# Optimization experiments

Measured on AMD Instinct MI355X. Metric: run time of the kernel, lower is better.

The kernel has to match this reference:

```python
import jax, jax.numpy as jnp
import numpy as np

N = 100_000   # nodes
E = 1_600_000 # edges (avg degree 16)
D0, D1, D2 = 128, 64, 64


def _linp(key, n_out, n_in):
    kw, kb = jax.random.split(key)
    s = 1.0 / np.sqrt(n_in)
    W = jax.random.uniform(kw, (n_out, n_in), jnp.float32, -s, s)
    b = jax.random.uniform(kb, (n_out,), jnp.float32, -s, s)
    return W, b


def setup_inputs() -> dict:
    key = jax.random.key(0)
    ks = jax.random.split(key, 9)
    h = jax.random.normal(ks[0], (N, D0), jnp.float32)
    # guarantee every row has at least one edge (avoids empty-row softmax / 0-std NaNs)
    rows = jnp.concatenate([jnp.arange(N, dtype=jnp.int32),
                            jax.random.randint(ks[1], (E - N,), 0, N, jnp.int32)])
    cols = jax.random.randint(ks[2], (E,), 0, N, jnp.int32)
    edge_index = jnp.stack([rows, cols])  # [2, E], row = softmax segment
    W11, b11 = _linp(ks[3], D1, D0)
    W12, b12 = _linp(ks[4], 1, D1)
    W13, b13 = _linp(ks[5], D1, D0)
    W21, b21 = _linp(ks[6], D2, D1)
    W22, b22 = _linp(ks[7], 1, D2)
    W23, b23 = _linp(ks[8], D2, D1)
    return dict(h=h, edge_index=edge_index,
                W11=W11, b11=b11, W12=W12, b12=b12, W13=W13, b13=b13,
                W21=W21, b21=b21, W22=W22, b22=b22, W23=W23, b23=b23)


def reference(h, edge_index, W11, b11, W12, b12, W13, b13,
              W21, b21, W22, b22, W23, b23):
    src, dst = edge_index[0], edge_index[1]

    def gat_layer(x, Wa, ba, We, be, Wv, bv):
        a = jnp.tanh(x @ Wa.T + ba)                       # [N, d] node scores (l11/l21)
        e = jnp.tanh((a[src] + a[dst]) @ We.T + be)[:, 0] # [E] per-edge logit (l12/l22)
        # per-row (segment) softmax over src = row index
        m = jax.ops.segment_max(e, src, num_segments=N)
        ex = jnp.exp(e - m[src])
        denom = jax.ops.segment_sum(ex, src, num_segments=N)
        att = ex / denom[src]                             # [E]
        v = jnp.tanh(x @ Wv.T + bv)                       # [N, d] values (l13/l23)
        out = jax.ops.segment_sum(att[:, None] * v[dst], src, num_segments=N)  # sparse mm
        return out / jnp.std(out, -1, keepdims=True, ddof=1)  # torch.std is unbiased

    h = gat_layer(h, W11, b11, W12, b12, W13, b13)
    h = gat_layer(h, W21, b21, W22, b22, W23, b23)
    return h
```

## Files before the change

kernel.cpp:

```cpp
#include <hip/hip_runtime.h>


#define WS_ALIGN 256
#define BIN_SHIFT 7
#define BIN_NODES 128
#define BIN_CAP 2560
#define MAX_BINS 1024
#define EPB 4096
#define AGGR_BLOCKS 2048

typedef __attribute__((ext_vector_type(8))) short short8;
typedef __attribute__((ext_vector_type(4))) short short4_t;
typedef __attribute__((ext_vector_type(4))) float f32x4;

__device__ __forceinline__ float fast_tanh(float x) {
  x = fminf(15.f, fmaxf(-15.f, x));
  float e = __expf(2.f * x);
  return (e - 1.f) * __builtin_amdgcn_rcpf(e + 1.f);
}

__device__ __forceinline__ unsigned short f32_to_bf16_rne(float f) {
  unsigned u = __float_as_uint(f);
  unsigned r = u + 0x7fffu + ((u >> 16) & 1u);
  return (unsigned short)(r >> 16);
}

__device__ __forceinline__ void prepw_one(const float* __restrict__ Wa,
                                          const float* __restrict__ Wv,
                                          short* __restrict__ Wh, short* __restrict__ Wl,
                                          int K, int i) {
  int KBLK = K / 32;
  int j = i & 7;
  int c = (i >> 3) & 15;
  int q = (i >> 7) & 3;
  int r = i >> 9;
  int nt = r / KBLK, kb = r - nt * KBLK;
  int row = nt * 16 + c;
  int col = kb * 32 + q * 8 + j;
  float f = (row < 64) ? Wa[row * K + col] : Wv[(row - 64) * K + col];
  unsigned u = __float_as_uint(f);
  float hf = __uint_as_float(u & 0xffff0000u);
  Wh[i] = (short)(u >> 16);
  Wl[i] = (short)(__float_as_uint(f - hf) >> 16);
}

__global__ void k_setup(const float* __restrict__ W11, const float* __restrict__ W13,
                        short* __restrict__ Wh1, short* __restrict__ Wl1,
                        const float* __restrict__ W21, const float* __restrict__ W23,
                        short* __restrict__ Wh2, short* __restrict__ Wl2,
                        int* __restrict__ cursor, int nb) {
  int i = blockIdx.x * 256 + threadIdx.x;
  if (i < 16384) {
    prepw_one(W11, W13, Wh1, Wl1, 128, i);
  } else if (i < 16384 + 8192) {
    prepw_one(W21, W23, Wh2, Wl2, 64, i - 16384);
  } else {
    int b = i - 24576;
    if (b < nb) cursor[b] = b * BIN_CAP;
  }
}

__global__ __launch_bounds__(256) void k_bin(const int* __restrict__ src,
                                             const int* __restrict__ dst,
                                             int* __restrict__ cursor,
                                             int* __restrict__ binned, int E, int nb) {
  __shared__ int ssrc[EPB];
  __shared__ int sdst[EPB];
  __shared__ int hist[MAX_BINS];
  __shared__ int base[MAX_BINS];
  int t = threadIdx.x;
  for (int i = t; i < nb; i += 256) hist[i] = 0;
  __syncthreads();
  int e0 = blockIdx.x * EPB;
  for (int i = t; i < EPB; i += 256) {
    int e = e0 + i;
    int sv = -1, dv = 0;
    if (e < E) {
      sv = src[e];
      dv = dst[e];
      atomicAdd(&hist[sv >> BIN_SHIFT], 1);
    }
    ssrc[i] = sv;
    sdst[i] = dv;
  }
  __syncthreads();
  for (int b = t; b < nb; b += 256) {
    int c = hist[b];
    base[b] = c ? atomicAdd(&cursor[b], c) : 0;
    hist[b] = 0;
  }
  __syncthreads();
  for (int i = t; i < EPB; i += 256) {
    int sv = ssrc[i];
    if (sv >= 0) {
      int b = sv >> BIN_SHIFT;
      int r = atomicAdd(&hist[b], 1);
      int pos = base[b] + r;
      if (pos < (b + 1) * BIN_CAP)
        binned[pos] = (sdst[i] << BIN_SHIFT) | (sv & (BIN_NODES - 1));
    }
  }
}

__global__ __launch_bounds__(256) void k_sort_bin(int* __restrict__ binned,
                                                  const int* __restrict__ cursor,
                                                  int* __restrict__ rs,
                                                  int* __restrict__ re, int n) {
  __shared__ int ents[BIN_CAP];
  __shared__ int sorted[BIN_CAP];
  __shared__ int hist[BIN_NODES];
  __shared__ int scan[BIN_NODES];
  __shared__ int cur[BIN_NODES];
  int bin = blockIdx.x;
  int t = threadIdx.x;
  int nbase = bin << BIN_SHIFT;
  int cnt = cursor[bin] - bin * BIN_CAP;
  if (cnt > BIN_CAP) cnt = BIN_CAP;
  if (t < BIN_NODES) hist[t] = 0;
  __syncthreads();
  int* bp = binned + (size_t)bin * BIN_CAP;
  for (int i = t; i < cnt; i += 256) {
    int pk = bp[i];
    ents[i] = pk;
    atomicAdd(&hist[pk & (BIN_NODES - 1)], 1);
  }
  __syncthreads();
  if (t < BIN_NODES) scan[t] = hist[t];
  __syncthreads();
  for (int off = 1; off < BIN_NODES; off <<= 1) {
    int add = (t < BIN_NODES && t >= off) ? scan[t - off] : 0;
    __syncthreads();
    if (t < BIN_NODES) scan[t] += add;
    __syncthreads();
  }
  if (t < BIN_NODES) {
    int ex = scan[t] - hist[t];
    cur[t] = ex;
    int node = nbase + t;
    if (node < n) {
      rs[node] = bin * BIN_CAP + ex;
      re[node] = bin * BIN_CAP + ex + hist[t];
    }
  }
  __syncthreads();
  for (int i = t; i < cnt; i += 256) {
    int pk = ents[i];
    int pos = atomicAdd(&cur[pk & (BIN_NODES - 1)], 1);
    sorted[pos] = pk;
  }
  __syncthreads();
  for (int i = t; i < cnt; i += 256) {
    int pk = sorted[i];
    int node = pk & (BIN_NODES - 1);
    int hi = scan[node];
    int lo = hi - hist[node];
    int r = lo;
    for (int j = lo; j < hi; j++) {
      int pj = sorted[j];
      r += (pj < pk) || (pj == pk && j < i);
    }
    ents[r] = pk >> BIN_SHIFT;
  }
  __syncthreads();
  for (int i = t; i < cnt; i += 256) bp[i] = ents[i];
}

template <int K>
__global__ __launch_bounds__(256) void k_node(
    const float* __restrict__ x, const short* __restrict__ Wh,
    const short* __restrict__ Wl, const float* __restrict__ ba,
    const float* __restrict__ we, const float* __restrict__ bv,
    unsigned short* __restrict__ v_out, float* __restrict__ s_out, int n) {
  constexpr int KBLK = K / 32;
  constexpr int RS = K + 8;
  __shared__ short sah[64 * RS];
  __shared__ short sal[64 * RS];
  __shared__ float sP[2][64];
  int t = threadIdx.x;
  int l = t & 63;
  int w = t >> 6;
  int q = l >> 4, c = l & 15;
  int node0b = blockIdx.x * 64;

  {
    const float4* xg = (const float4*)(x + (size_t)node0b * K);
    constexpr int R4 = K / 4;
#pragma unroll
    for (int it = 0; it < 64 * R4 / 256; it++) {
      int i = it * 256 + t;
      int r = i / R4, k4 = i - r * R4;
      float4 val = (node0b + r < n) ? xg[i] : (float4){0.f, 0.f, 0.f, 0.f};
      float xv[4] = {val.x, val.y, val.z, val.w};
      short4_t hi, lo;
#pragma unroll
      for (int j = 0; j < 4; j++) {
        unsigned u = __float_as_uint(xv[j]);
        hi[j] = (short)(u >> 16);
        float hf = __uint_as_float(u & 0xffff0000u);
        lo[j] = (short)(__float_as_uint(xv[j] - hf) >> 16);
      }
      *(short4_t*)&sah[r * RS + k4 * 4] = hi;
      *(short4_t*)&sal[r * RS + k4 * 4] = lo;
    }
  }

  const short8* WhF = (const short8*)Wh;
  const short8* WlF = (const short8*)Wl;
  short8 wfh[2][KBLK], wfl[2][KBLK];
#pragma unroll
  for (int mt = 0; mt < 2; mt++)
#pragma unroll
    for (int kb = 0; kb < KBLK; kb++) {
      size_t f = (size_t)((2 * w + mt) * KBLK + kb) * 64 + l;
      wfh[mt][kb] = WhF[f];
      wfl[mt][kb] = WlF[f];
    }
  __syncthreads();

  f32x4 acc[4][2];
#pragma unroll
  for (int ns = 0; ns < 4; ns++)
#pragma unroll
    for (int mt = 0; mt < 2; mt++) acc[ns][mt] = (f32x4){0.f, 0.f, 0.f, 0.f};

#pragma unroll
  for (int ns = 0; ns < 4; ns++) {
#pragma unroll
    for (int kb = 0; kb < KBLK; kb++) {
      int off = (ns * 16 + c) * RS + kb * 32 + q * 8;
      short8 ah = *(const short8*)&sah[off];
      short8 al = *(const short8*)&sal[off];
#pragma unroll
      for (int mt = 0; mt < 2; mt++) {
        acc[ns][mt] = __builtin_amdgcn_mfma_f32_16x16x32_bf16(ah, wfh[mt][kb], acc[ns][mt], 0, 0, 0);
        acc[ns][mt] = __builtin_amdgcn_mfma_f32_16x16x32_bf16(ah, wfl[mt][kb], acc[ns][mt], 0, 0, 0);
        acc[ns][mt] = __builtin_amdgcn_mfma_f32_16x16x32_bf16(al, wfh[mt][kb], acc[ns][mt], 0, 0, 0);
      }
    }
  }

  if (w < 2) {
    float bav0 = ba[w * 32 + c], wev0 = we[w * 32 + c];
    float bav1 = ba[w * 32 + 16 + c], wev1 = we[w * 32 + 16 + c];
#pragma unroll
    for (int ns = 0; ns < 4; ns++) {
#pragma unroll
      for (int r = 0; r < 4; r++) {
        float pv = fast_tanh(acc[ns][0][r] + bav0) * wev0 +
                   fast_tanh(acc[ns][1][r] + bav1) * wev1;
#pragma unroll
        for (int mm = 1; mm < 16; mm <<= 1) pv += __shfl_xor(pv, mm, 64);
        if (c == 0) sP[w][ns * 16 + q * 4 + r] = pv;
      }
    }
  } else {
    int wv = w - 2;
    float bvv0 = bv[wv * 32 + c], bvv1 = bv[wv * 32 + 16 + c];
#pragma unroll
    for (int ns = 0; ns < 4; ns++) {
#pragma unroll
      for (int r = 0; r < 4; r++) {
        int node = node0b + ns * 16 + q * 4 + r;
        if (node < n) {
          v_out[(size_t)node * 64 + wv * 32 + c] =
              f32_to_bf16_rne(fast_tanh(acc[ns][0][r] + bvv0));
          v_out[(size_t)node * 64 + wv * 32 + 16 + c] =
              f32_to_bf16_rne(fast_tanh(acc[ns][1][r] + bvv1));
        }
      }
    }
  }
  __syncthreads();
  if (t < 64) {
    int node = node0b + t;
    if (node < n) s_out[node] = sP[0][t] + sP[1][t];
  }
}

__global__ __launch_bounds__(256) void k_aggr(const int* __restrict__ rs,
                                              const int* __restrict__ re,
                                              const int* __restrict__ col,
                                              const float* __restrict__ s,
                                              const float* __restrict__ be_p,
                                              const unsigned short* __restrict__ v,
                                              float* __restrict__ out, int n) {
  int wid = (int)((blockIdx.x * 256 + threadIdx.x) >> 6);
  int nw = AGGR_BLOCKS * 4;
  int l = threadIdx.x & 63;
  int q = l >> 4;
  int g = l & 15;
  int qb = l & 48;
  float be = be_p[0];
  int ngroups = (n + 3) >> 2;
  if (wid >= ngroups) return;

  int pnode = wid * 4 + q;
  bool pvn = pnode < n;
  int pe0 = pvn ? rs[pnode] : 0;
  int pe1 = pvn ? re[pnode] : 0;
  float psrow = pvn ? s[pnode] : 0.f;
  int pc;
  float psc;
  {
    int prem = pe1 - pe0;
    pc = (g < prem) ? col[pe0 + g] : 0;
    psc = (g < prem) ? s[pc] : 0.f;
  }

  for (int grp = wid; grp < ngroups; grp += nw) {
    int e0 = pe0, e1 = pe1;
    float srow = psrow;
    int c0 = pc;
    float sc0 = psc;
    int nxt = grp + nw;
    if (nxt < ngroups) {
      int nn = nxt * 4 + q;
      bool nv = nn < n;
      pe0 = nv ? rs[nn] : 0;
      pe1 = nv ? re[nn] : 0;
      psrow = nv ? s[nn] : 0.f;
    }
    int m = e1 - e0;
    float a0 = 0.f, a1 = 0.f, a2 = 0.f, a3 = 0.f;
    float dl = 0.f;

    {
      float w = (g < m) ? __expf(fast_tanh(srow + sc0 + be)) : 0.f;
      dl += w;
#pragma unroll
      for (int jj = 0; jj < 16; jj++) {
        int cj = __shfl(c0, qb + jj, 64);
        float wj = __shfl(w, qb + jj, 64);
        uint2 pk = *(const uint2*)(v + ((size_t)cj << 6) + (g << 2));
        a0 = fmaf(wj, __uint_as_float(pk.x << 16), a0);
        a1 = fmaf(wj, __uint_as_float(pk.x & 0xffff0000u), a1);
        a2 = fmaf(wj, __uint_as_float(pk.y << 16), a2);
        a3 = fmaf(wj, __uint_as_float(pk.y & 0xffff0000u), a3);
      }
    }
    if (nxt < ngroups) {
      int nrem = pe1 - pe0;
      pc = (g < nrem) ? col[pe0 + g] : 0;
      psc = (g < nrem) ? s[pc] : 0.f;
    }
    for (int cb = 16; !__all(m - cb <= 0); cb += 16) {
      bool act = (cb + g) < m;
      int c = act ? col[e0 + cb + g] : 0;
      float w = act ? __expf(fast_tanh(srow + s[c] + be)) : 0.f;
      dl += w;
#pragma unroll
      for (int jj = 0; jj < 16; jj++) {
        int cj = __shfl(c, qb + jj, 64);
        float wj = __shfl(w, qb + jj, 64);
        uint2 pk = *(const uint2*)(v + ((size_t)cj << 6) + (g << 2));
        a0 = fmaf(wj, __uint_as_float(pk.x << 16), a0);
        a1 = fmaf(wj, __uint_as_float(pk.x & 0xffff0000u), a1);
        a2 = fmaf(wj, __uint_as_float(pk.y << 16), a2);
        a3 = fmaf(wj, __uint_as_float(pk.y & 0xffff0000u), a3);
      }
    }

#pragma unroll
    for (int mm = 1; mm < 16; mm <<= 1) dl += __shfl_xor(dl, mm, 64);
    float inv = __builtin_amdgcn_rcpf(dl);
    float o0 = a0 * inv, o1 = a1 * inv, o2 = a2 * inv, o3 = a3 * inv;
    float t0 = o0 + o1 + o2 + o3;
    float t1 = o0 * o0 + o1 * o1 + o2 * o2 + o3 * o3;
#pragma unroll
    for (int mm = 1; mm < 16; mm <<= 1) {
      t0 += __shfl_xor(t0, mm, 64);
      t1 += __shfl_xor(t1, mm, 64);
    }
    float var = (t1 - t0 * t0 * (1.0f / 64.f)) * (1.0f / 63.f);
    float isd = __builtin_amdgcn_rsqf(var);
    int cnode = grp * 4 + q;
    if (cnode < n) {
      float4 r = {o0 * isd, o1 * isd, o2 * isd, o3 * isd};
      *(float4*)&out[(size_t)cnode * 64 + (g << 2)] = r;
    }
  }
}

extern "C" void kernel_launch(void* const* d_in, const int* in_sizes, int n_in,
                              void* d_out, int out_size, void* d_ws, size_t ws_size,
                              hipStream_t stream) {
  const float* h = (const float*)d_in[0];
  const int* ei = (const int*)d_in[1];
  const float* W11 = (const float*)d_in[2];
  const float* b11 = (const float*)d_in[3];
  const float* W12 = (const float*)d_in[4];
  const float* b12 = (const float*)d_in[5];
  const float* W13 = (const float*)d_in[6];
  const float* b13 = (const float*)d_in[7];
  const float* W21 = (const float*)d_in[8];
  const float* b21 = (const float*)d_in[9];
  const float* W22 = (const float*)d_in[10];
  const float* b22 = (const float*)d_in[11];
  const float* W23 = (const float*)d_in[12];
  const float* b23 = (const float*)d_in[13];

  const int N = in_sizes[0] / 128;
  const int E = in_sizes[1] / 2;
  const int* src = ei;
  const int* dst = ei + E;
  const int NB = (N + BIN_NODES - 1) >> BIN_SHIFT;

  char* p = (char*)d_ws;
  auto alloc = [&](size_t bytes) -> void* {
    void* r = (void*)p;
    p += (bytes + WS_ALIGN - 1) / WS_ALIGN * WS_ALIGN;
    return r;
  };
  int* cursor = (int*)alloc((size_t)NB * 4);
  int* binned = (int*)alloc((size_t)NB * BIN_CAP * 4);
  int* rsb = (int*)alloc((size_t)N * 4);
  int* reb = (int*)alloc((size_t)N * 4);
  float* sbuf = (float*)alloc((size_t)N * 4);
  unsigned short* vbuf = (unsigned short*)alloc((size_t)N * 64 * 2);
  float* out1 = (float*)alloc((size_t)N * 64 * 4);
  short* Wh1 = (short*)alloc(128 * 128 * 2);
  short* Wl1 = (short*)alloc(128 * 128 * 2);
  short* Wh2 = (short*)alloc(128 * 64 * 2);
  short* Wl2 = (short*)alloc(128 * 64 * 2);

  k_setup<<<(24576 + NB + 255) / 256, 256, 0, stream>>>(
      W11, W13, Wh1, Wl1, W21, W23, Wh2, Wl2, cursor, NB);

  k_bin<<<(E + EPB - 1) / EPB, 256, 0, stream>>>(src, dst, cursor, binned, E, NB);
  k_sort_bin<<<NB, 256, 0, stream>>>(binned, cursor, rsb, reb, N);

  k_node<128><<<(N + 63) / 64, 256, 0, stream>>>(h, Wh1, Wl1, b11, W12, b13, vbuf, sbuf, N);
  k_aggr<<<AGGR_BLOCKS, 256, 0, stream>>>(rsb, reb, binned, sbuf, b12, vbuf, out1, N);

  k_node<64><<<(N + 63) / 64, 256, 0, stream>>>(out1, Wh2, Wl2, b21, W22, b23, vbuf, sbuf, N);
  k_aggr<<<AGGR_BLOCKS, 256, 0, stream>>>(rsb, reb, binned, sbuf, b22, vbuf, (float*)d_out, N);
}
```

Measured before the change: 280.4 us.

## Batch all neighbor value gathers up front in aggregation kernel, prefetch two edge chunks

The aggregation kernel now issues all 16 (or 32, when any row has more than 16 edges) bf16 value-row gathers into registers before doing any arithmetic. Previously loads and FMAs were interleaved one edge at a time. Each node's first two 16-edge chunks of column indices and scores are prefetched for the next group. The grid is halved, occupancy is hinted with launch_bounds(256,4), and the stride now comes from gridDim. This aims for more memory-level parallelism on the random gathers, at the cost of more registers (32 uint2 arrays) and fewer resident waves.

```diff
diff --git a/kernel.cpp b/kernel.cpp
--- a/kernel.cpp
+++ b/kernel.cpp
@@ -7,7 +7,7 @@
 #define BIN_CAP 2560
 #define MAX_BINS 1024
 #define EPB 4096
-#define AGGR_BLOCKS 2048
+#define AGGR_BLOCKS 1024
 
 typedef __attribute__((ext_vector_type(8))) short short8;
 typedef __attribute__((ext_vector_type(4))) short short4_t;
@@ -277,15 +277,15 @@
   }
 }
 
-__global__ __launch_bounds__(256) void k_aggr(const int* __restrict__ rs,
-                                              const int* __restrict__ re,
-                                              const int* __restrict__ col,
-                                              const float* __restrict__ s,
-                                              const float* __restrict__ be_p,
-                                              const unsigned short* __restrict__ v,
-                                              float* __restrict__ out, int n) {
+__global__ __launch_bounds__(256, 4) void k_aggr(const int* __restrict__ rs,
+                                                 const int* __restrict__ re,
+                                                 const int* __restrict__ col,
+                                                 const float* __restrict__ s,
+                                                 const float* __restrict__ be_p,
+                                                 const unsigned short* __restrict__ v,
+                                                 float* __restrict__ out, int n) {
   int wid = (int)((blockIdx.x * 256 + threadIdx.x) >> 6);
-  int nw = AGGR_BLOCKS * 4;
+  int nwv = (int)gridDim.x * 4;
   int l = threadIdx.x & 63;
   int q = l >> 4;
   int g = l & 15;
@@ -294,64 +294,89 @@
   int ngroups = (n + 3) >> 2;
   if (wid >= ngroups) return;
 
-  int pnode = wid * 4 + q;
-  bool pvn = pnode < n;
-  int pe0 = pvn ? rs[pnode] : 0;
-  int pe1 = pvn ? re[pnode] : 0;
-  float psrow = pvn ? s[pnode] : 0.f;
-  int pc;
-  float psc;
+  int ce0, ce1;
+  float csrow, csc0, csc1;
+  int cc0, cc1;
   {
-    int prem = pe1 - pe0;
-    pc = (g < prem) ? col[pe0 + g] : 0;
-    psc = (g < prem) ? s[pc] : 0.f;
-  }
-
-  for (int grp = wid; grp < ngroups; grp += nw) {
-    int e0 = pe0, e1 = pe1;
-    float srow = psrow;
-    int c0 = pc;
-    float sc0 = psc;
-    int nxt = grp + nw;
+    int node = wid * 4 + q;
+    bool vn = node < n;
+    ce0 = vn ? rs[node] : 0;
+    ce1 = vn ? re[node] : 0;
+    csrow = vn ? s[node] : 0.f;
+    int m = ce1 - ce0;
+    cc0 = (g < m) ? col[ce0 + g] : 0;
+    cc1 = (g + 16 < m) ? col[ce0 + g + 16] : 0;
+    csc0 = (g < m) ? s[cc0] : 0.f;
+    csc1 = (g + 16 < m) ? s[cc1] : 0.f;
+  }
+
+  for (int grp = wid; grp < ngroups; grp += nwv) {
+    int m = ce1 - ce0;
+    int e0 = ce0;
+    float srow = csrow;
+    bool two = __any(m > 16);
+
+    uint2 pv[16];
+#pragma unroll
+    for (int jj = 0; jj < 16; jj++) {
+      int cj = __shfl(cc0, qb + jj, 64);
+      pv[jj] = *(const uint2*)(v + ((size_t)cj << 6) + (g << 2));
+    }
+    uint2 pw[16];
+    if (two) {
+#pragma unroll
+      for (int jj = 0; jj < 16; jj++) {
+        int cj = __shfl(cc1, qb + jj, 64);
+        pw[jj] = *(const uint2*)(v + ((size_t)cj << 6) + (g << 2));
+      }
+    }
+
+    float w0 = (g < m) ? __expf(fast_tanh(srow + csc0 + be)) : 0.f;
+    float w1 = (g + 16 < m) ? __expf(fast_tanh(srow + csc1 + be)) : 0.f;
+    float dl = w0 + w1;
+
+    int nxt = grp + nwv;
     if (nxt < ngroups) {
-      int nn = nxt * 4 + q;
-      bool nv = nn < n;
-      pe0 = nv ? rs[nn] : 0;
-      pe1 = nv ? re[nn] : 0;
-      psrow = nv ? s[nn] : 0.f;
-    }
-    int m = e1 - e0;
+      int node = nxt * 4 + q;
+      bool vn = node < n;
+      ce0 = vn ? rs[node] : 0;
+      ce1 = vn ? re[node] : 0;
+      csrow = vn ? s[node] : 0.f;
+      int nm = ce1 - ce0;
+      cc0 = (g < nm) ? col[ce0 + g] : 0;
+      cc1 = (g + 16 < nm) ? col[ce0 + g + 16] : 0;
+      csc0 = (g < nm) ? s[cc0] : 0.f;
+      csc1 = (g + 16 < nm) ? s[cc1] : 0.f;
+    }
+
     float a0 = 0.f, a1 = 0.f, a2 = 0.f, a3 = 0.f;
-    float dl = 0.f;
-
-    {
-      float w = (g < m) ? __expf(fast_tanh(srow + sc0 + be)) : 0.f;
-      dl += w;
+#pragma unroll
+    for (int jj = 0; jj < 16; jj++) {
+      float wj = __shfl(w0, qb + jj, 64);
+      a0 = fmaf(wj, __uint_as_float(pv[jj].x << 16), a0);
+      a1 = fmaf(wj, __uint_as_float(pv[jj].x & 0xffff0000u), a1);
+      a2 = fmaf(wj, __uint_as_float(pv[jj].y << 16), a2);
+      a3 = fmaf(wj, __uint_as_float(pv[jj].y & 0xffff0000u), a3);
+    }
+    if (two) {
 #pragma unroll
       for (int jj = 0; jj < 16; jj++) {
-        int cj = __shfl(c0, qb + jj, 64);
-        float wj = __shfl(w, qb + jj, 64);
-        uint2 pk = *(const uint2*)(v + ((size_t)cj << 6) + (g << 2));
-        a0 = fmaf(wj, __uint_as_float(pk.x << 16), a0);
-        a1 = fmaf(wj, __uint_as_float(pk.x & 0xffff0000u), a1);
-        a2 = fmaf(wj, __uint_as_float(pk.y << 16), a2);
-        a3 = fmaf(wj, __uint_as_float(pk.y & 0xffff0000u), a3);
-      }
-    }
-    if (nxt < ngroups) {
-      int nrem = pe1 - pe0;
-      pc = (g < nrem) ? col[pe0 + g] : 0;
-      psc = (g < nrem) ? s[pc] : 0.f;
-    }
-    for (int cb = 16; !__all(m - cb <= 0); cb += 16) {
+        float wj = __shfl(w1, qb + jj, 64);
+        a0 = fmaf(wj, __uint_as_float(pw[jj].x << 16), a0);
+        a1 = fmaf(wj, __uint_as_float(pw[jj].x & 0xffff0000u), a1);
+        a2 = fmaf(wj, __uint_as_float(pw[jj].y << 16), a2);
+        a3 = fmaf(wj, __uint_as_float(pw[jj].y & 0xffff0000u), a3);
+      }
+    }
+    for (int cb = 32; !__all(m - cb <= 0); cb += 16) {
       bool act = (cb + g) < m;
       int c = act ? col[e0 + cb + g] : 0;
-      float w = act ? __expf(fast_tanh(srow + s[c] + be)) : 0.f;
-      dl += w;
+      float wx = act ? __expf(fast_tanh(srow + s[c] + be)) : 0.f;
+      dl += wx;
 #pragma unroll
       for (int jj = 0; jj < 16; jj++) {
         int cj = __shfl(c, qb + jj, 64);
-        float wj = __shfl(w, qb + jj, 64);
+        float wj = __shfl(wx, qb + jj, 64);
         uint2 pk = *(const uint2*)(v + ((size_t)cj << 6) + (g << 2));
         a0 = fmaf(wj, __uint_as_float(pk.x << 16), a0);
         a1 = fmaf(wj, __uint_as_float(pk.x & 0xffff0000u), a1);
```

After: 300.1 us. 7.0% more time.

## Stage per-strip edge weights in shared memory for segment-softmax aggregation

Applied to the files above, without the earlier changes.

The aggregation kernel now gives each block a strip of 32 consecutive nodes. It first computes every edge's softmax weight and column index cooperatively into shared memory, with per-node denominators. Each wave then gathers value rows for 8 nodes, splitting each node's edges across four 16-lane slices and reducing with cross-lane shuffles. This replaces the persistent grid-stride loop with its register prefetching and per-edge shuffle broadcasts. It adds block barriers and serial per-node loops (row-score fill and denominator sum), and silently truncates strips whose edge count exceeds the shared capacity.

```diff
diff --git a/kernel.cpp b/kernel.cpp
--- a/kernel.cpp
+++ b/kernel.cpp
@@ -7,7 +7,7 @@
 #define BIN_CAP 2560
 #define MAX_BINS 1024
 #define EPB 4096
-#define AGGR_BLOCKS 2048
+#define STRIP_CAP 1024
 
 typedef __attribute__((ext_vector_type(8))) short short8;
 typedef __attribute__((ext_vector_type(4))) short short4_t;
@@ -284,85 +284,76 @@
                                               const float* __restrict__ be_p,
                                               const unsigned short* __restrict__ v,
                                               float* __restrict__ out, int n) {
-  int wid = (int)((blockIdx.x * 256 + threadIdx.x) >> 6);
-  int nw = AGGR_BLOCKS * 4;
-  int l = threadIdx.x & 63;
-  int q = l >> 4;
+  __shared__ float wle[STRIP_CAP];
+  __shared__ int cle[STRIP_CAP];
+  __shared__ float srw[STRIP_CAP];
+  __shared__ int lrs[32];
+  __shared__ int lre[32];
+  __shared__ float sden[32];
+  int t = threadIdx.x;
+  int strip0 = blockIdx.x * 32;
+  if (strip0 >= n) return;
+
+  int estart = rs[strip0];
+  int ecnt = re[strip0 + 31] - estart;
+  if (ecnt > STRIP_CAP) ecnt = STRIP_CAP;
+
+  if (t < 32) {
+    int a = rs[strip0 + t] - estart;
+    int b = re[strip0 + t] - estart;
+    if (a > STRIP_CAP) a = STRIP_CAP;
+    if (b > STRIP_CAP) b = STRIP_CAP;
+    lrs[t] = a;
+    lre[t] = b;
+  }
+  __syncthreads();
+  if (t < 32) {
+    float sv = s[strip0 + t];
+    for (int i = lrs[t]; i < lre[t]; i++) srw[i] = sv;
+  }
+  __syncthreads();
+  float be = be_p[0];
+  for (int i = t; i < ecnt; i += 256) {
+    int c = col[estart + i];
+    cle[i] = c;
+    wle[i] = __expf(fast_tanh(srw[i] + s[c] + be));
+  }
+  __syncthreads();
+  if (t < 32) {
+    float d = 0.f;
+    for (int i = lrs[t]; i < lre[t]; i++) d += wle[i];
+    sden[t] = d;
+  }
+  __syncthreads();
+
+  int wv_ = t >> 6;
+  int l = t & 63;
+  int es = l >> 4;
   int g = l & 15;
-  int qb = l & 48;
-  float be = be_p[0];
-  int ngroups = (n + 3) >> 2;
-  if (wid >= ngroups) return;
-
-  int pnode = wid * 4 + q;
-  bool pvn = pnode < n;
-  int pe0 = pvn ? rs[pnode] : 0;
-  int pe1 = pvn ? re[pnode] : 0;
-  float psrow = pvn ? s[pnode] : 0.f;
-  int pc;
-  float psc;
-  {
-    int prem = pe1 - pe0;
-    pc = (g < prem) ? col[pe0 + g] : 0;
-    psc = (g < prem) ? s[pc] : 0.f;
-  }
-
-  for (int grp = wid; grp < ngroups; grp += nw) {
-    int e0 = pe0, e1 = pe1;
-    float srow = psrow;
-    int c0 = pc;
-    float sc0 = psc;
-    int nxt = grp + nw;
-    if (nxt < ngroups) {
-      int nn = nxt * 4 + q;
-      bool nv = nn < n;
-      pe0 = nv ? rs[nn] : 0;
-      pe1 = nv ? re[nn] : 0;
-      psrow = nv ? s[nn] : 0.f;
-    }
-    int m = e1 - e0;
+#pragma unroll 1
+  for (int j = 0; j < 8; j++) {
+    int nd = wv_ * 8 + j;
+    int b0 = lrs[nd];
+    int m = lre[nd] - b0;
     float a0 = 0.f, a1 = 0.f, a2 = 0.f, a3 = 0.f;
-    float dl = 0.f;
-
-    {
-      float w = (g < m) ? __expf(fast_tanh(srow + sc0 + be)) : 0.f;
-      dl += w;
-#pragma unroll
-      for (int jj = 0; jj < 16; jj++) {
-        int cj = __shfl(c0, qb + jj, 64);
-        float wj = __shfl(w, qb + jj, 64);
-        uint2 pk = *(const uint2*)(v + ((size_t)cj << 6) + (g << 2));
-        a0 = fmaf(wj, __uint_as_float(pk.x << 16), a0);
-        a1 = fmaf(wj, __uint_as_float(pk.x & 0xffff0000u), a1);
-        a2 = fmaf(wj, __uint_as_float(pk.y << 16), a2);
-        a3 = fmaf(wj, __uint_as_float(pk.y & 0xffff0000u), a3);
-      }
-    }
-    if (nxt < ngroups) {
-      int nrem = pe1 - pe0;
-      pc = (g < nrem) ? col[pe0 + g] : 0;
-      psc = (g < nrem) ? s[pc] : 0.f;
-    }
-    for (int cb = 16; !__all(m - cb <= 0); cb += 16) {
-      bool act = (cb + g) < m;
-      int c = act ? col[e0 + cb + g] : 0;
-      float w = act ? __expf(fast_tanh(srow + s[c] + be)) : 0.f;
-      dl += w;
-#pragma unroll
-      for (int jj = 0; jj < 16; jj++) {
-        int cj = __shfl(c, qb + jj, 64);
-        float wj = __shfl(w, qb + jj, 64);
-        uint2 pk = *(const uint2*)(v + ((size_t)cj << 6) + (g << 2));
-        a0 = fmaf(wj, __uint_as_float(pk.x << 16), a0);
-        a1 = fmaf(wj, __uint_as_float(pk.x & 0xffff0000u), a1);
-        a2 = fmaf(wj, __uint_as_float(pk.y << 16), a2);
-        a3 = fmaf(wj, __uint_as_float(pk.y & 0xffff0000u), a3);
-      }
-    }
-
-#pragma unroll
-    for (int mm = 1; mm < 16; mm <<= 1) dl += __shfl_xor(dl, mm, 64);
-    float inv = __builtin_amdgcn_rcpf(dl);
+    for (int k = es; k < m; k += 4) {
+      int idx = b0 + k;
+      int c = cle[idx];
+      float wj = wle[idx];
+      uint2 pk = *(const uint2*)(v + ((size_t)c << 6) + (g << 2));
+      a0 = fmaf(wj, __uint_as_float(pk.x << 16), a0);
+      a1 = fmaf(wj, __uint_as_float(pk.x & 0xffff0000u), a1);
+      a2 = fmaf(wj, __uint_as_float(pk.y << 16), a2);
+      a3 = fmaf(wj, __uint_as_float(pk.y & 0xffff0000u), a3);
+    }
+#pragma unroll
+    for (int mm = 16; mm < 64; mm <<= 1) {
+      a0 += __shfl_xor(a0, mm, 64);
+      a1 += __shfl_xor(a1, mm, 64);
+      a2 += __shfl_xor(a2, mm, 64);
+      a3 += __shfl_xor(a3, mm, 64);
+    }
+    float inv = __builtin_amdgcn_rcpf(sden[nd]);
     float o0 = a0 * inv, o1 = a1 * inv, o2 = a2 * inv, o3 = a3 * inv;
     float t0 = o0 + o1 + o2 + o3;
     float t1 = o0 * o0 + o1 * o1 + o2 * o2 + o3 * o3;
@@ -373,10 +364,9 @@
     }
     float var = (t1 - t0 * t0 * (1.0f / 64.f)) * (1.0f / 63.f);
     float isd = __builtin_amdgcn_rsqf(var);
-    int cnode = grp * 4 + q;
-    if (cnode < n) {
+    if (es == 0) {
       float4 r = {o0 * isd, o1 * isd, o2 * isd, o3 * isd};
-      *(float4*)&out[(size_t)cnode * 64 + (g << 2)] = r;
+      *(float4*)&out[(size_t)(strip0 + nd) * 64 + (g << 2)] = r;
     }
   }
 }
@@ -430,8 +420,8 @@
   k_sort_bin<<<NB, 256, 0, stream>>>(binned, cursor, rsb, reb, N);
 
   k_node<128><<<(N + 63) / 64, 256, 0, stream>>>(h, Wh1, Wl1, b11, W12, b13, vbuf, sbuf, N);
-  k_aggr<<<AGGR_BLOCKS, 256, 0, stream>>>(rsb, reb, binned, sbuf, b12, vbuf, out1, N);
+  k_aggr<<<NB * 4, 256, 0, stream>>>(rsb, reb, binned, sbuf, b12, vbuf, out1, N);
 
   k_node<64><<<(N + 63) / 64, 256, 0, stream>>>(out1, Wh2, Wl2, b21, W22, b23, vbuf, sbuf, N);
-  k_aggr<<<AGGR_BLOCKS, 256, 0, stream>>>(rsb, reb, binned, sbuf, b22, vbuf, (float*)d_out, N);
-}
+  k_aggr<<<NB * 4, 256, 0, stream>>>(rsb, reb, binned, sbuf, b22, vbuf, (float*)d_out, N);
+}
```

After: 295.3 us. +5.3%, slower.
